# Kernel optimization log

Measured on AMD Instinct MI355X. Metric: run time of the kernel, lower is better.

## Reference

```python
import jax, jax.numpy as jnp
import numpy as np

NEG = -10000.0
SLOPE = 0.2


def setup_inputs() -> dict:
    key = jax.random.key(0)
    k1, k2, k3, k4, k5 = jax.random.split(key, 5)
    B, N, F_in, F_out = 8, 2048, 512, 512
    text = jax.random.normal(k1, (B, N, F_in), dtype=jnp.float32)
    adj = jax.random.randint(k2, (B, N, N), 0, 2, dtype=jnp.int32)
    sc = 1.0 / np.sqrt(F_in)
    W = jax.random.normal(k3, (F_in, F_out), dtype=jnp.float32) * sc
    b = jnp.zeros((F_out,), dtype=jnp.float32)
    a_src = jax.random.normal(k4, (F_out,), dtype=jnp.float32) * sc
    a_dst = jax.random.normal(k5, (F_out,), dtype=jnp.float32) * sc
    return {"text": text, "adj": adj, "W": W, "b": b, "a_src": a_src, "a_dst": a_dst}


def reference(text, adj, W, b, a_src, a_dst):
    # hidden: [B, N, F_out]
    hidden = jnp.einsum("bnf,fo->bno", text, W) + b
    s = jnp.einsum("bno,o->bn", hidden, a_src)  # src score per node
    d = jnp.einsum("bno,o->bn", hidden, a_dst)  # dst score per node
    scores = s[:, :, None] + d[:, None, :]      # [B, N, N]
    scores = jnp.where(scores >= 0, scores, SLOPE * scores)  # LeakyReLU
    # faithful to original: masked_fill where adj.bool() is True
    scores = jnp.where(adj.astype(bool), NEG, scores)
    attn = jax.nn.softmax(scores, axis=-1)
    return jnp.einsum("bnm,bmo->bno", attn, hidden)
```

## Files before the change

### kernel.cpp

```cpp
#include <hip/hip_runtime.h>
#include <stdint.h>

#define NB 8
#define NN 2048
#define NF 512
#define TOTN (NB * NN)

typedef unsigned short u16;
typedef short bf16x8 __attribute__((ext_vector_type(8)));
typedef float f32x4 __attribute__((ext_vector_type(4)));

__device__ __forceinline__ u16 f2bf(float x) {
  unsigned u = __float_as_uint(x);
  unsigned r = 0x7FFFu + ((u >> 16) & 1u);
  return (u16)((u + r) >> 16);
}

__device__ __forceinline__ void gl2lds16(const void* g, void* l) {
  __builtin_amdgcn_global_load_lds((const __attribute__((address_space(1))) void*)g,
                                   (__attribute__((address_space(3))) void*)l,
                                   16, 0, 0);
}

__global__ __launch_bounds__(256) void conv_kernel(
    const float* __restrict__ text, const float* __restrict__ W,
    u16* __restrict__ text_bf, u16* __restrict__ Wt) {
  int blk = blockIdx.x;
  if (blk < 8192) {
    int idx = blk * 256 + threadIdx.x;
    float4 v = ((const float4*)text)[idx];
    ushort4 o;
    o.x = f2bf(v.x); o.y = f2bf(v.y); o.z = f2bf(v.z); o.w = f2bf(v.w);
    ((ushort4*)text_bf)[idx] = o;
  } else {
    int t = (blk - 8192) * 256 + threadIdx.x;
    int o = t >> 9, f = t & 511;
    Wt[o * NF + f] = f2bf(W[f * NF + o]);
  }
}

__global__ __launch_bounds__(256) void gemm1_kernel(
    const u16* __restrict__ A,
    const u16* __restrict__ Bt,
    const float* __restrict__ bias, const float* __restrict__ a_src,
    const float* __restrict__ a_dst, u16* __restrict__ hT,
    float* __restrict__ s, float* __restrict__ d) {
  __shared__ u16 Alds[128 * 32];
  __shared__ u16 Blds[128 * 32];

  const int bn = blockIdx.x, bm = blockIdx.y;
  const int t = threadIdx.x, wave = t >> 6, lane = t & 63;
  const int wm = (wave >> 1) * 64, wn = (wave & 1) * 64;

  f32x4 acc[4][4];
#pragma unroll
  for (int i = 0; i < 4; ++i)
#pragma unroll
    for (int j = 0; j < 4; ++j) acc[i][j] = (f32x4){0.f, 0.f, 0.f, 0.f};

  const int rowA0 = bm * 128, rowB0 = bn * 128;
  const int srow = (lane >> 2);
  const int scol = (lane & 3) * 8;

  for (int kt = 0; kt < NF; kt += 32) {
#pragma unroll
    for (int q = 0; q < 2; ++q) {
      int r = wave * 32 + q * 16;
      gl2lds16(A + (size_t)(rowA0 + r + srow) * NF + (kt + scol), &Alds[r * 32]);
    }
#pragma unroll
    for (int q = 0; q < 2; ++q) {
      int r = wave * 32 + q * 16;
      gl2lds16(Bt + (size_t)(rowB0 + r + srow) * NF + (kt + scol), &Blds[r * 32]);
    }
    __syncthreads();

    const int fr = lane & 15;
    const int k0 = (lane >> 4) * 8;
    bf16x8 af[4], bfr[4];
#pragma unroll
    for (int i = 0; i < 4; ++i)
      af[i] = *(const bf16x8*)&Alds[(wm + i * 16 + fr) * 32 + k0];
#pragma unroll
    for (int j = 0; j < 4; ++j)
      bfr[j] = *(const bf16x8*)&Blds[(wn + j * 16 + fr) * 32 + k0];
#pragma unroll
    for (int i = 0; i < 4; ++i)
#pragma unroll
      for (int j = 0; j < 4; ++j)
        acc[i][j] = __builtin_amdgcn_mfma_f32_16x16x32_bf16(af[i], bfr[j],
                                                            acc[i][j], 0, 0, 0);
    __syncthreads();
  }

  const int quad = lane >> 4, ln16 = lane & 15;
  float sa[4] = {0.f, 0.f, 0.f, 0.f}, da[4] = {0.f, 0.f, 0.f, 0.f};
#pragma unroll
  for (int i = 0; i < 4; ++i) {
    int m0 = bm * 128 + wm + i * 16 + quad * 4;
#pragma unroll
    for (int r = 0; r < 4; ++r) {
      int m = m0 + r;
      float bv = bias[m];
      float asv = a_src[m], adv = a_dst[m];
#pragma unroll
      for (int j = 0; j < 4; ++j) {
        int n = bn * 128 + wn + j * 16 + ln16;
        float h = acc[i][j][r] + bv;
        hT[(size_t)m * TOTN + n] = f2bf(h);
        sa[j] = fmaf(h, asv, sa[j]);
        da[j] = fmaf(h, adv, da[j]);
      }
    }
  }
#pragma unroll
  for (int j = 0; j < 4; ++j) {
    float v = sa[j] + __shfl_xor(sa[j], 16, 64);
    v += __shfl_xor(v, 32, 64);
    float w2 = da[j] + __shfl_xor(da[j], 16, 64);
    w2 += __shfl_xor(w2, 32, 64);
    if (quad == 0) {
      int n = bn * 128 + wn + j * 16 + ln16;
      atomicAdd(&s[n], v);
      atomicAdd(&d[n], w2);
    }
  }
}

__global__ __launch_bounds__(256, 4) void fused_attn_kernel(
    const int* __restrict__ adj, const float* __restrict__ s,
    const float* __restrict__ d, const u16* __restrict__ hT,
    float* __restrict__ out) {
  __shared__ u16 Plds[2 * 512];
  __shared__ u16 Blds[16 * 512];
  __shared__ float lpart[32 * 8];
  __shared__ float linv_lds[32];

  const int z = blockIdx.z;
  const int oh = blockIdx.y;
  const int i0 = blockIdx.x * 32;
  const int o0 = oh * 256;
  const int t = threadIdx.x, wave = t >> 6, lane = t & 63;
  const int quad = lane >> 4, ln16 = lane & 15;

  const int pr = t >> 3;
  const int pj = (t & 7) * 4;
  const float si = s[z * NN + i0 + pr];
  const int* arow = adj + (size_t)(z * NN + i0 + pr) * NN;
  const float* db = d + z * NN;

  const int sr = lane >> 2;
  const int sq = (lane & 3) ^ ((sr >> 1) & 3);

  f32x4 acc[2][4];
#pragma unroll
  for (int i = 0; i < 2; ++i)
#pragma unroll
    for (int j = 0; j < 4; ++j) acc[i][j] = (f32x4){0.f, 0.f, 0.f, 0.f};

  int4 a0 = *(const int4*)&arow[pj];
  float4 dv0 = *(const float4*)&db[pj];
  int4 a1 = *(const int4*)&arow[32 + pj];
  float4 dv1 = *(const float4*)&db[32 + pj];

  float lsum = 0.f;
  const int fslot = ln16 * 4 + (quad ^ ((ln16 >> 1) & 3));

  for (int kt = 0; kt < NN; kt += 32) {
    float x0 = si + dv0.x, x1 = si + dv0.y, x2 = si + dv0.z, x3 = si + dv0.w;
    x0 = fmaxf(x0, 0.2f * x0); x1 = fmaxf(x1, 0.2f * x1);
    x2 = fmaxf(x2, 0.2f * x2); x3 = fmaxf(x3, 0.2f * x3);
    float p0 = a0.x ? 0.f : __expf(x0);
    float p1 = a0.y ? 0.f : __expf(x1);
    float p2 = a0.z ? 0.f : __expf(x2);
    float p3 = a0.w ? 0.f : __expf(x3);
    lsum += (p0 + p1) + (p2 + p3);
    ushort4 pk;
    pk.x = f2bf(p0); pk.y = f2bf(p1); pk.z = f2bf(p2); pk.w = f2bf(p3);

    __syncthreads();

    {
      int rc = pr & 15, ch = pr >> 4;
      int slot = rc * 4 + ((pj >> 3) ^ ((rc >> 1) & 3));
      *(ushort4*)((char*)Plds + ch * 1024 + slot * 16 + (pj & 7) * 2) = pk;
    }
#pragma unroll
    for (int c = 0; c < 4; ++c) {
      int ch = c * 4 + wave;
      gl2lds16(hT + (size_t)(o0 + ch * 16 + sr) * TOTN + z * NN + kt + sq * 8,
               &Blds[ch * 512]);
    }
    __syncthreads();

    a0 = a1; dv0 = dv1;
    if (kt + 64 < NN) {
      a1 = *(const int4*)&arow[kt + 64 + pj];
      dv1 = *(const float4*)&db[kt + 64 + pj];
    }

    bf16x8 af[2], bfr[4];
#pragma unroll
    for (int i = 0; i < 2; ++i)
      af[i] = *(const bf16x8*)((const char*)Plds + i * 1024 + fslot * 16);
#pragma unroll
    for (int j = 0; j < 4; ++j) {
      int ch = (wave * 64 + j * 16) >> 4;
      bfr[j] = *(const bf16x8*)((const char*)Blds + ch * 1024 + fslot * 16);
    }
#pragma unroll
    for (int i = 0; i < 2; ++i)
#pragma unroll
      for (int j = 0; j < 4; ++j)
        acc[i][j] = __builtin_amdgcn_mfma_f32_16x16x32_bf16(af[i], bfr[j],
                                                            acc[i][j], 0, 0, 0);
  }

  lpart[pr * 8 + (t & 7)] = lsum;
  __syncthreads();
  if (t < 32) {
    const float* lp = &lpart[t * 8];
    float tot = ((lp[0] + lp[1]) + (lp[2] + lp[3])) +
                ((lp[4] + lp[5]) + (lp[6] + lp[7]));
    linv_lds[t] = 1.0f / tot;
  }
  __syncthreads();

#pragma unroll
  for (int i = 0; i < 2; ++i) {
#pragma unroll
    for (int r = 0; r < 4; ++r) {
      int m = i * 16 + quad * 4 + r;
      float sc = linv_lds[m];
      size_t base = (size_t)(z * NN + i0 + m) * NF;
#pragma unroll
      for (int j = 0; j < 4; ++j) {
        int o = o0 + wave * 64 + j * 16 + ln16;
        out[base + o] = acc[i][j][r] * sc;
      }
    }
  }
}

extern "C" void kernel_launch(void* const* d_in, const int* in_sizes, int n_in,
                              void* d_out, int out_size, void* d_ws,
                              size_t ws_size, hipStream_t stream) {
  const float* text  = (const float*)d_in[0];
  const int*   adj   = (const int*)d_in[1];
  const float* W     = (const float*)d_in[2];
  const float* bias  = (const float*)d_in[3];
  const float* a_src = (const float*)d_in[4];
  const float* a_dst = (const float*)d_in[5];
  float* out = (float*)d_out;

  char* ws = (char*)d_ws;
  u16*   text_bf = (u16*)(ws + 0);
  u16*   Wt      = (u16*)(ws + 16777216);
  u16*   hT      = (u16*)(ws + 17301504);
  float* s       = (float*)(ws + 34078720);
  float* d       = (float*)(ws + 34144256);

  hipMemsetAsync(s, 0, 131072, stream);

  conv_kernel<<<9216, 256, 0, stream>>>(text, W, text_bf, Wt);

  gemm1_kernel<<<dim3(128, 4, 1), 256, 0, stream>>>(Wt, text_bf, bias, a_src,
                                                    a_dst, hT, s, d);

  fused_attn_kernel<<<dim3(NN / 32, 2, NB), 256, 0, stream>>>(adj, s, d, hT, out);
}
```

Before: 351.3 us.

## Pack adjacency into bitmask, pre-swizzle hidden tiles, enlarge attention row tile

Adds a pre-pass that packs the int32 adjacency matrix into one bit per entry. The attention kernel then reads 32x less mask data. gemm1 now writes hidden directly in a tiled, swizzled slab layout, so each attention K-step loads one contiguous 16 KB block. The attention kernel processes 64 rows and 64 keys per iteration instead of 32x32, doubling reuse of each B tile, at the cost of more registers and lower occupancy (launch bounds 4 to 2). The extra pack kernel still reads the full adjacency once.

```diff
diff --git a/kernel.cpp b/kernel.cpp
--- a/kernel.cpp
+++ b/kernel.cpp
@@ -21,6 +21,7 @@
                                    (__attribute__((address_space(3))) void*)l,
                                    16, 0, 0);
 }
+
 
 __global__ __launch_bounds__(256) void conv_kernel(
     const float* __restrict__ text, const float* __restrict__ W,
@@ -39,16 +40,32 @@
   }
 }
 
+__global__ __launch_bounds__(256) void pack_kernel(
+    const int* __restrict__ adj, uint32_t* __restrict__ bm) {
+  int gid = blockIdx.x * 256 + threadIdx.x;
+  const int4* p = (const int4*)(adj + (size_t)gid * 32);
+  uint32_t bits = 0;
+#pragma unroll
+  for (int c = 0; c < 8; ++c) {
+    int4 a = p[c];
+    bits |= (uint32_t)(a.x != 0) << (c * 4 + 0);
+    bits |= (uint32_t)(a.y != 0) << (c * 4 + 1);
+    bits |= (uint32_t)(a.z != 0) << (c * 4 + 2);
+    bits |= (uint32_t)(a.w != 0) << (c * 4 + 3);
+  }
+  bm[gid] = bits;
+}
+
 __global__ __launch_bounds__(256) void gemm1_kernel(
     const u16* __restrict__ A,
     const u16* __restrict__ Bt,
     const float* __restrict__ bias, const float* __restrict__ a_src,
-    const float* __restrict__ a_dst, u16* __restrict__ hT,
+    const float* __restrict__ a_dst, u16* __restrict__ hS,
     float* __restrict__ s, float* __restrict__ d) {
   __shared__ u16 Alds[128 * 32];
   __shared__ u16 Blds[128 * 32];
 
-  const int bn = blockIdx.x, bm = blockIdx.y;
+  const int bn = blockIdx.x, bm_ = blockIdx.y;
   const int t = threadIdx.x, wave = t >> 6, lane = t & 63;
   const int wm = (wave >> 1) * 64, wn = (wave & 1) * 64;
 
@@ -58,7 +75,7 @@
 #pragma unroll
     for (int j = 0; j < 4; ++j) acc[i][j] = (f32x4){0.f, 0.f, 0.f, 0.f};
 
-  const int rowA0 = bm * 128, rowB0 = bn * 128;
+  const int rowA0 = bm_ * 128, rowB0 = bn * 128;
   const int srow = (lane >> 2);
   const int scol = (lane & 3) * 8;
 
@@ -97,17 +114,24 @@
   float sa[4] = {0.f, 0.f, 0.f, 0.f}, da[4] = {0.f, 0.f, 0.f, 0.f};
 #pragma unroll
   for (int i = 0; i < 4; ++i) {
-    int m0 = bm * 128 + wm + i * 16 + quad * 4;
+    int m0 = bm_ * 128 + wm + i * 16 + quad * 4;
 #pragma unroll
     for (int r = 0; r < 4; ++r) {
       int m = m0 + r;
       float bv = bias[m];
       float asv = a_src[m], adv = a_dst[m];
+      int oh = m >> 8, och = (m >> 4) & 15, rc = m & 15;
 #pragma unroll
       for (int j = 0; j < 4; ++j) {
         int n = bn * 128 + wn + j * 16 + ln16;
         float h = acc[i][j][r] + bv;
-        hT[(size_t)m * TOTN + n] = f2bf(h);
+        int zz = n >> 11, nz = n & 2047;
+        int kc = nz >> 5, kin = nz & 31;
+        size_t off = ((((size_t)zz * 2 + oh) * 64 + kc) << 13)
+                     + (och << 9)
+                     + ((size_t)(rc * 4 + ((kin >> 3) ^ ((rc >> 1) & 3))) << 3)
+                     + (kin & 7);
+        hS[off] = f2bf(h);
         sa[j] = fmaf(h, asv, sa[j]);
         da[j] = fmaf(h, adv, da[j]);
       }
@@ -127,117 +151,123 @@
   }
 }
 
-__global__ __launch_bounds__(256, 4) void fused_attn_kernel(
-    const int* __restrict__ adj, const float* __restrict__ s,
-    const float* __restrict__ d, const u16* __restrict__ hT,
+__global__ __launch_bounds__(256, 2) void fused_attn_kernel(
+    const uint32_t* __restrict__ bm, const float* __restrict__ s,
+    const float* __restrict__ d, const u16* __restrict__ hS,
     float* __restrict__ out) {
-  __shared__ u16 Plds[2 * 512];
-  __shared__ u16 Blds[16 * 512];
-  __shared__ float lpart[32 * 8];
-  __shared__ float linv_lds[32];
-
-  const int z = blockIdx.z;
-  const int oh = blockIdx.y;
-  const int i0 = blockIdx.x * 32;
-  const int o0 = oh * 256;
+  __shared__ u16 Blds[16384];
+  __shared__ u16 Plds[4096];
+  __shared__ float lpart[256];
+  __shared__ float linv_lds[64];
+
+  const int z = blockIdx.z, oh = blockIdx.y;
+  const int i0 = blockIdx.x * 64;
   const int t = threadIdx.x, wave = t >> 6, lane = t & 63;
   const int quad = lane >> 4, ln16 = lane & 15;
 
-  const int pr = t >> 3;
-  const int pj = (t & 7) * 4;
+  const int pr = t >> 2;
+  const int ko = (t & 3) * 16;
   const float si = s[z * NN + i0 + pr];
-  const int* arow = adj + (size_t)(z * NN + i0 + pr) * NN;
+  const uint32_t* bmrow = bm + (size_t)(z * NN + i0 + pr) * 64;
   const float* db = d + z * NN;
 
-  const int sr = lane >> 2;
-  const int sq = (lane & 3) ^ ((sr >> 1) & 3);
-
-  f32x4 acc[2][4];
-#pragma unroll
-  for (int i = 0; i < 2; ++i)
+  const char* slabB = (const char*)hS + (size_t)(z * 2 + oh) * 1048576;
+
+  f32x4 acc[4][4];
+#pragma unroll
+  for (int i = 0; i < 4; ++i)
 #pragma unroll
     for (int j = 0; j < 4; ++j) acc[i][j] = (f32x4){0.f, 0.f, 0.f, 0.f};
 
-  int4 a0 = *(const int4*)&arow[pj];
-  float4 dv0 = *(const float4*)&db[pj];
-  int4 a1 = *(const int4*)&arow[32 + pj];
-  float4 dv1 = *(const float4*)&db[32 + pj];
+  uint32_t bw = bmrow[ko >> 5];
+  float4 dv[4];
+#pragma unroll
+  for (int c = 0; c < 4; ++c) dv[c] = *(const float4*)&db[ko + c * 4];
+
+  const int fslot = ln16 * 4 + (quad ^ ((ln16 >> 1) & 3));
+  const int prc = pr & 15, pch = pr >> 4;
+  const int ph = ko >> 5, pq0 = (ko >> 3) & 3;
+  char* pbase = (char*)Plds + ph * 4096 + pch * 1024;
+  char* pdst0 = pbase + (prc * 4 + (pq0 ^ ((prc >> 1) & 3))) * 16;
+  char* pdst1 = pbase + (prc * 4 + ((pq0 + 1) ^ ((prc >> 1) & 3))) * 16;
 
   float lsum = 0.f;
-  const int fslot = ln16 * 4 + (quad ^ ((ln16 >> 1) & 3));
-
-  for (int kt = 0; kt < NN; kt += 32) {
-    float x0 = si + dv0.x, x1 = si + dv0.y, x2 = si + dv0.z, x3 = si + dv0.w;
-    x0 = fmaxf(x0, 0.2f * x0); x1 = fmaxf(x1, 0.2f * x1);
-    x2 = fmaxf(x2, 0.2f * x2); x3 = fmaxf(x3, 0.2f * x3);
-    float p0 = a0.x ? 0.f : __expf(x0);
-    float p1 = a0.y ? 0.f : __expf(x1);
-    float p2 = a0.z ? 0.f : __expf(x2);
-    float p3 = a0.w ? 0.f : __expf(x3);
-    lsum += (p0 + p1) + (p2 + p3);
-    ushort4 pk;
-    pk.x = f2bf(p0); pk.y = f2bf(p1); pk.z = f2bf(p2); pk.w = f2bf(p3);
+
+  for (int kt = 0; kt < NN; kt += 64) {
+    uint32_t bits16 = (bw >> (ko & 16)) & 0xFFFFu;
+    u16 pk[16];
+#pragma unroll
+    for (int cc = 0; cc < 4; ++cc) {
+      float4 dq = dv[cc];
+#pragma unroll
+      for (int e = 0; e < 4; ++e) {
+        float dj = (e == 0) ? dq.x : (e == 1) ? dq.y : (e == 2) ? dq.z : dq.w;
+        float x = si + dj;
+        float xm = fmaxf(x, 0.2f * x);
+        float p = ((bits16 >> (cc * 4 + e)) & 1u) ? 0.f : __expf(xm);
+        lsum += p;
+        pk[cc * 4 + e] = f2bf(p);
+      }
+    }
 
     __syncthreads();
 
+    *(int4*)pdst0 = *(int4*)&pk[0];
+    *(int4*)pdst1 = *(int4*)&pk[8];
+
     {
-      int rc = pr & 15, ch = pr >> 4;
-      int slot = rc * 4 + ((pj >> 3) ^ ((rc >> 1) & 3));
-      *(ushort4*)((char*)Plds + ch * 1024 + slot * 16 + (pj & 7) * 2) = pk;
-    }
-#pragma unroll
-    for (int c = 0; c < 4; ++c) {
-      int ch = c * 4 + wave;
-      gl2lds16(hT + (size_t)(o0 + ch * 16 + sr) * TOTN + z * NN + kt + sq * 8,
-               &Blds[ch * 512]);
+      const char* gB = slabB + (size_t)kt * 512;
+#pragma unroll
+      for (int c = 0; c < 8; ++c) {
+        int boff = (c * 4 + wave) * 1024;
+        gl2lds16(gB + boff + lane * 16, (char*)Blds + boff);
+      }
     }
     __syncthreads();
 
-    a0 = a1; dv0 = dv1;
     if (kt + 64 < NN) {
-      a1 = *(const int4*)&arow[kt + 64 + pj];
-      dv1 = *(const float4*)&db[kt + 64 + pj];
-    }
-
-    bf16x8 af[2], bfr[4];
-#pragma unroll
-    for (int i = 0; i < 2; ++i)
-      af[i] = *(const bf16x8*)((const char*)Plds + i * 1024 + fslot * 16);
-#pragma unroll
-    for (int j = 0; j < 4; ++j) {
-      int ch = (wave * 64 + j * 16) >> 4;
-      bfr[j] = *(const bf16x8*)((const char*)Blds + ch * 1024 + fslot * 16);
-    }
-#pragma unroll
-    for (int i = 0; i < 2; ++i)
+      bw = bmrow[((kt + 64) >> 5) + (ko >> 5)];
+#pragma unroll
+      for (int c = 0; c < 4; ++c)
+        dv[c] = *(const float4*)&db[kt + 64 + ko + c * 4];
+    }
+
+#pragma unroll
+    for (int h = 0; h < 2; ++h) {
+      bf16x8 af[4], bfv[4];
+#pragma unroll
+      for (int i = 0; i < 4; ++i)
+        af[i] = *(const bf16x8*)((const char*)Plds + h * 4096 + i * 1024 + fslot * 16);
 #pragma unroll
       for (int j = 0; j < 4; ++j)
-        acc[i][j] = __builtin_amdgcn_mfma_f32_16x16x32_bf16(af[i], bfr[j],
-                                                            acc[i][j], 0, 0, 0);
-  }
-
-  lpart[pr * 8 + (t & 7)] = lsum;
+        bfv[j] = *(const bf16x8*)((const char*)Blds + h * 16384 +
+                                  (wave * 4 + j) * 1024 + fslot * 16);
+#pragma unroll
+      for (int i = 0; i < 4; ++i)
+#pragma unroll
+        for (int j = 0; j < 4; ++j)
+          acc[i][j] = __builtin_amdgcn_mfma_f32_16x16x32_bf16(af[i], bfv[j],
+                                                              acc[i][j], 0, 0, 0);
+    }
+  }
+
+  lpart[pr * 4 + (t & 3)] = lsum;
   __syncthreads();
-  if (t < 32) {
-    const float* lp = &lpart[t * 8];
-    float tot = ((lp[0] + lp[1]) + (lp[2] + lp[3])) +
-                ((lp[4] + lp[5]) + (lp[6] + lp[7]));
-    linv_lds[t] = 1.0f / tot;
+  if (t < 64) {
+    const float* lp = &lpart[t * 4];
+    linv_lds[t] = 1.0f / ((lp[0] + lp[1]) + (lp[2] + lp[3]));
   }
   __syncthreads();
 
 #pragma unroll
-  for (int i = 0; i < 2; ++i) {
+  for (int i = 0; i < 4; ++i) {
 #pragma unroll
     for (int r = 0; r < 4; ++r) {
       int m = i * 16 + quad * 4 + r;
       float sc = linv_lds[m];
-      size_t base = (size_t)(z * NN + i0 + m) * NF;
-#pragma unroll
-      for (int j = 0; j < 4; ++j) {
-        int o = o0 + wave * 64 + j * 16 + ln16;
-        out[base + o] = acc[i][j][r] * sc;
-      }
+      float* ob = out + ((size_t)(z * NN) + i0 + m) * NF + oh * 256 + wave * 64;
+#pragma unroll
+      for (int j = 0; j < 4; ++j) ob[j * 16 + ln16] = acc[i][j][r] * sc;
     }
   }
 }
@@ -254,18 +284,21 @@
   float* out = (float*)d_out;
 
   char* ws = (char*)d_ws;
-  u16*   text_bf = (u16*)(ws + 0);
-  u16*   Wt      = (u16*)(ws + 16777216);
-  u16*   hT      = (u16*)(ws + 17301504);
-  float* s       = (float*)(ws + 34078720);
-  float* d       = (float*)(ws + 34144256);
+  u16*      text_bf = (u16*)(ws + 0);
+  u16*      Wt      = (u16*)(ws + 16777216);
+  u16*      hS      = (u16*)(ws + 17301504);
+  float*    s       = (float*)(ws + 34078720);
+  float*    d       = (float*)(ws + 34144256);
+  uint32_t* bmask   = (uint32_t*)(ws + 34209792);
 
   hipMemsetAsync(s, 0, 131072, stream);
 
   conv_kernel<<<9216, 256, 0, stream>>>(text, W, text_bf, Wt);
+  pack_kernel<<<4096, 256, 0, stream>>>(adj, bmask);
 
   gemm1_kernel<<<dim3(128, 4, 1), 256, 0, stream>>>(Wt, text_bf, bias, a_src,
-                                                    a_dst, hT, s, d);
-
-  fused_attn_kernel<<<dim3(NN / 32, 2, NB), 256, 0, stream>>>(adj, s, d, hT, out);
-}
+                                                    a_dst, hS, s, d);
+
+  fused_attn_kernel<<<dim3(NN / 64, 2, NB), 256, 0, stream>>>(bmask, s, d, hS,
+                                                              out);
+}
```

Result: faster. 301.4 us (-14.2%).
